# Performance work log

Measured on AMD Instinct MI355X. Metric: run time of the kernel, lower is better.

## Reference

```python
import jax, jax.numpy as jnp
import numpy as np

NNODES = 8192
DIM = 256
ALPHA = 3.0
NEG_SLOPE = 0.2


def setup_inputs() -> dict:
    key = jax.random.key(0)
    k1, k2, k3, k4 = jax.random.split(key, 4)
    return {
        "idx": jnp.arange(NNODES, dtype=jnp.int64) if jax.config.jax_enable_x64 else jnp.arange(NNODES, dtype=jnp.int32),
        "emb1_w": jax.random.normal(k1, (NNODES, DIM), dtype=jnp.float32),
        "emb2_w": jax.random.normal(k2, (NNODES, DIM), dtype=jnp.float32),
        "att_w": jax.random.normal(k3, (2 * DIM,), dtype=jnp.float32) * (1.0 / np.sqrt(2 * DIM)),
        "att_b": jax.random.normal(k4, (1,), dtype=jnp.float32),
    }


def reference(idx, emb1_w, emb2_w, att_w, att_b):
    # Embedding lookup + tanh(alpha * v)
    v1 = jnp.tanh(ALPHA * emb1_w[idx])  # [N, D]
    v2 = jnp.tanh(ALPHA * emb2_w[idx])  # [N, D]
    # Linear(cat(v1_i, v2_j)) decomposes exactly into an outer sum of two
    # per-node projections (same math, no N x N x 2D intermediate).
    s1 = v1 @ att_w[:DIM]  # [N]
    s2 = v2 @ att_w[DIM:]  # [N]
    scores = s1[:, None] + s2[None, :] + att_b[0]  # [N, N]
    scores = jax.nn.leaky_relu(scores, negative_slope=NEG_SLOPE)
    weights = jax.nn.softmax(scores, axis=1)  # row softmax
    # adj[i, idx] = weights[i]  (vectorized column scatter)
    n = idx.shape[0]
    adj = jnp.zeros((n, n), dtype=weights.dtype).at[:, idx].set(weights)
    return adj
```

## Files before the change

kernel.cpp:

```cpp
#include <hip/hip_runtime.h>
#include <math.h>

#define NNODES 8192
#define DIM 256
#define ALPHA 3.0f
#define SLOPE 0.2f
#define LOG2E 1.4426950408889634f

typedef float floatx4 __attribute__((ext_vector_type(4)));

__global__ __launch_bounds__(256) void s_kernel(
    const int* __restrict__ idx,
    const float* __restrict__ e1, const float* __restrict__ e2,
    const float* __restrict__ w,
    float* __restrict__ s1, float* __restrict__ s2)
{
    const int waveId = threadIdx.x >> 6;
    const int lane   = threadIdx.x & 63;
    const int node   = (blockIdx.x << 2) + waveId;
    const int row    = idx[node];

    const float4* e1v = (const float4*)(e1 + (size_t)row * DIM);
    const float4* e2v = (const float4*)(e2 + (size_t)row * DIM);
    const float4* w1v = (const float4*)w;
    const float4* w2v = (const float4*)(w + DIM);

    float4 a  = e1v[lane];
    float4 b  = e2v[lane];
    float4 w1 = w1v[lane];
    float4 w2 = w2v[lane];

    float acc1 = tanhf(ALPHA * a.x) * w1.x + tanhf(ALPHA * a.y) * w1.y
               + tanhf(ALPHA * a.z) * w1.z + tanhf(ALPHA * a.w) * w1.w;
    float acc2 = tanhf(ALPHA * b.x) * w2.x + tanhf(ALPHA * b.y) * w2.y
               + tanhf(ALPHA * b.z) * w2.z + tanhf(ALPHA * b.w) * w2.w;

    #pragma unroll
    for (int off = 32; off > 0; off >>= 1) {
        acc1 += __shfl_down(acc1, off);
        acc2 += __shfl_down(acc2, off);
    }
    if (lane == 0) {
        s1[node] = acc1;
        s2[node] = acc2;
    }
}

__global__ __launch_bounds__(256) void row_kernel(
    const float* __restrict__ s1, const float* __restrict__ s2,
    const int* __restrict__ idx, const float* __restrict__ att_b,
    float* __restrict__ out)
{
    __shared__ float lds[8];
    const int t    = threadIdx.x;
    const int lane = t & 63;
    const int wv   = t >> 6;
    const int row  = blockIdx.x;

    const int4*   idxv = (const int4*)idx;
    const float4* s2v  = (const float4*)s2;
    int4   iv[8];
    float4 v[8];
    float lmax = -3.402823466e38f;
    #pragma unroll
    for (int k = 0; k < 8; ++k) {
        iv[k] = idxv[k * 256 + t];
        v[k]  = s2v[k * 256 + t];
        lmax = fmaxf(lmax, fmaxf(fmaxf(v[k].x, v[k].y), fmaxf(v[k].z, v[k].w)));
    }

    #pragma unroll
    for (int off = 32; off > 0; off >>= 1)
        lmax = fmaxf(lmax, __shfl_xor(lmax, off));
    if (lane == 0) lds[wv] = lmax;
    __syncthreads();
    const float s2max = fmaxf(fmaxf(lds[0], lds[1]), fmaxf(lds[2], lds[3]));

    const float base = s1[row] + att_b[0];
    const float tm   = base + s2max;
    const float m    = fmaxf(tm, SLOPE * tm);
    const float mexp = m * LOG2E;

    float e[32];
    float dsum = 0.0f;
    #pragma unroll
    for (int k = 0; k < 8; ++k) {
        float x0 = base + v[k].x, x1 = base + v[k].y;
        float x2 = base + v[k].z, x3 = base + v[k].w;
        x0 = fmaxf(x0, SLOPE * x0);
        x1 = fmaxf(x1, SLOPE * x1);
        x2 = fmaxf(x2, SLOPE * x2);
        x3 = fmaxf(x3, SLOPE * x3);
        e[4 * k + 0] = __builtin_amdgcn_exp2f(fmaf(x0, LOG2E, -mexp));
        e[4 * k + 1] = __builtin_amdgcn_exp2f(fmaf(x1, LOG2E, -mexp));
        e[4 * k + 2] = __builtin_amdgcn_exp2f(fmaf(x2, LOG2E, -mexp));
        e[4 * k + 3] = __builtin_amdgcn_exp2f(fmaf(x3, LOG2E, -mexp));
        dsum += (e[4 * k + 0] + e[4 * k + 1]) + (e[4 * k + 2] + e[4 * k + 3]);
    }

    #pragma unroll
    for (int off = 32; off > 0; off >>= 1)
        dsum += __shfl_xor(dsum, off);
    if (lane == 0) lds[4 + wv] = dsum;
    __syncthreads();
    const float denom = (lds[4] + lds[5]) + (lds[6] + lds[7]);
    const float inv = 1.0f / denom;

    float* orow = out + (size_t)row * NNODES;
    #pragma unroll
    for (int k = 0; k < 8; ++k) {
        floatx4 r;
        r.x = e[4 * k + 0] * inv;
        r.y = e[4 * k + 1] * inv;
        r.z = e[4 * k + 2] * inv;
        r.w = e[4 * k + 3] * inv;
        const int c0 = (k * 256 + t) * 4;
        if (iv[k].x == c0 && iv[k].y == c0 + 1 && iv[k].z == c0 + 2 && iv[k].w == c0 + 3) {
            __builtin_nontemporal_store(r, (floatx4*)(orow + c0));
        } else {
            orow[iv[k].x] = r.x;
            orow[iv[k].y] = r.y;
            orow[iv[k].z] = r.z;
            orow[iv[k].w] = r.w;
        }
    }
}

extern "C" void kernel_launch(void* const* d_in, const int* in_sizes, int n_in,
                              void* d_out, int out_size, void* d_ws, size_t ws_size,
                              hipStream_t stream) {
    const int*   idx   = (const int*)d_in[0];
    const float* emb1  = (const float*)d_in[1];
    const float* emb2  = (const float*)d_in[2];
    const float* att_w = (const float*)d_in[3];
    const float* att_b = (const float*)d_in[4];
    float* out = (float*)d_out;

    float* s1 = (float*)d_ws;
    float* s2 = s1 + NNODES;

    s_kernel<<<NNODES / 4, 256, 0, stream>>>(idx, emb1, emb2, att_w, s1, s2);
    row_kernel<<<NNODES, 256, 0, stream>>>(s1, s2, idx, att_b, out);
}
```

Measured before the change: 292.0 us.

## Process multiple rows per block, reusing s2 max and identity-index check

Each block of the row kernel now handles eight output rows. It loads s2 and idx once, computes the global s2 max once, and does a block-wide check of whether idx is the identity permutation. That check selects a uniform vectorized nontemporal store path and removes the per-element index registers. The aim is to amortize redundant loads and reductions across rows, at the cost of fewer blocks and a serialized loop of per-row barriers, while the kernel stays bound by output writes.

Result: no change. 293.8 us (+0.6%).

```diff
diff --git a/kernel.cpp b/kernel.cpp
--- a/kernel.cpp
+++ b/kernel.cpp
@@ -6,6 +6,7 @@
 #define ALPHA 3.0f
 #define SLOPE 0.2f
 #define LOG2E 1.4426950408889634f
+#define ROWS_PER_BLOCK 8
 
 typedef float floatx4 __attribute__((ext_vector_type(4)));
 
@@ -51,77 +52,94 @@
     const int* __restrict__ idx, const float* __restrict__ att_b,
     float* __restrict__ out)
 {
-    __shared__ float lds[8];
+    __shared__ float red[8];
+    __shared__ float rmax[4];
+    __shared__ int   rok[4];
     const int t    = threadIdx.x;
     const int lane = t & 63;
     const int wv   = t >> 6;
-    const int row  = blockIdx.x;
+    const int row0 = blockIdx.x * ROWS_PER_BLOCK;
 
-    const int4*   idxv = (const int4*)idx;
-    const float4* s2v  = (const float4*)s2;
-    int4   iv[8];
+    const float4* s2v = (const float4*)s2;
     float4 v[8];
     float lmax = -3.402823466e38f;
+    int ok = 1;
+    {
+        const int4* idxv = (const int4*)idx;
+        #pragma unroll
+        for (int k = 0; k < 8; ++k) {
+            v[k] = s2v[k * 256 + t];
+            lmax = fmaxf(lmax, fmaxf(fmaxf(v[k].x, v[k].y), fmaxf(v[k].z, v[k].w)));
+            int4 iv = idxv[k * 256 + t];
+            const int c0 = (k * 256 + t) * 4;
+            ok &= (iv.x == c0) & (iv.y == c0 + 1) & (iv.z == c0 + 2) & (iv.w == c0 + 3);
+        }
+    }
     #pragma unroll
-    for (int k = 0; k < 8; ++k) {
-        iv[k] = idxv[k * 256 + t];
-        v[k]  = s2v[k * 256 + t];
-        lmax = fmaxf(lmax, fmaxf(fmaxf(v[k].x, v[k].y), fmaxf(v[k].z, v[k].w)));
+    for (int off = 32; off > 0; off >>= 1) {
+        lmax = fmaxf(lmax, __shfl_xor(lmax, off));
+        ok &= __shfl_xor(ok, off);
     }
-
-    #pragma unroll
-    for (int off = 32; off > 0; off >>= 1)
-        lmax = fmaxf(lmax, __shfl_xor(lmax, off));
-    if (lane == 0) lds[wv] = lmax;
+    if (lane == 0) { rmax[wv] = lmax; rok[wv] = ok; }
     __syncthreads();
-    const float s2max = fmaxf(fmaxf(lds[0], lds[1]), fmaxf(lds[2], lds[3]));
-
-    const float base = s1[row] + att_b[0];
-    const float tm   = base + s2max;
-    const float m    = fmaxf(tm, SLOPE * tm);
-    const float mexp = m * LOG2E;
+    const float s2max = fmaxf(fmaxf(rmax[0], rmax[1]), fmaxf(rmax[2], rmax[3]));
+    const int   okAll = rok[0] & rok[1] & rok[2] & rok[3];
+    const float bb    = att_b[0];
 
     float e[32];
-    float dsum = 0.0f;
-    #pragma unroll
-    for (int k = 0; k < 8; ++k) {
-        float x0 = base + v[k].x, x1 = base + v[k].y;
-        float x2 = base + v[k].z, x3 = base + v[k].w;
-        x0 = fmaxf(x0, SLOPE * x0);
-        x1 = fmaxf(x1, SLOPE * x1);
-        x2 = fmaxf(x2, SLOPE * x2);
-        x3 = fmaxf(x3, SLOPE * x3);
-        e[4 * k + 0] = __builtin_amdgcn_exp2f(fmaf(x0, LOG2E, -mexp));
-        e[4 * k + 1] = __builtin_amdgcn_exp2f(fmaf(x1, LOG2E, -mexp));
-        e[4 * k + 2] = __builtin_amdgcn_exp2f(fmaf(x2, LOG2E, -mexp));
-        e[4 * k + 3] = __builtin_amdgcn_exp2f(fmaf(x3, LOG2E, -mexp));
-        dsum += (e[4 * k + 0] + e[4 * k + 1]) + (e[4 * k + 2] + e[4 * k + 3]);
-    }
+    for (int r = 0; r < ROWS_PER_BLOCK; ++r) {
+        const int row   = row0 + r;
+        const float base = s1[row] + bb;
+        const float tm   = base + s2max;
+        const float m    = fmaxf(tm, SLOPE * tm);
+        const float mexp = m * LOG2E;
 
-    #pragma unroll
-    for (int off = 32; off > 0; off >>= 1)
-        dsum += __shfl_xor(dsum, off);
-    if (lane == 0) lds[4 + wv] = dsum;
-    __syncthreads();
-    const float denom = (lds[4] + lds[5]) + (lds[6] + lds[7]);
-    const float inv = 1.0f / denom;
+        float dsum = 0.0f;
+        #pragma unroll
+        for (int k = 0; k < 8; ++k) {
+            float x0 = base + v[k].x, x1 = base + v[k].y;
+            float x2 = base + v[k].z, x3 = base + v[k].w;
+            x0 = fmaxf(x0, SLOPE * x0);
+            x1 = fmaxf(x1, SLOPE * x1);
+            x2 = fmaxf(x2, SLOPE * x2);
+            x3 = fmaxf(x3, SLOPE * x3);
+            e[4 * k + 0] = __builtin_amdgcn_exp2f(fmaf(x0, LOG2E, -mexp));
+            e[4 * k + 1] = __builtin_amdgcn_exp2f(fmaf(x1, LOG2E, -mexp));
+            e[4 * k + 2] = __builtin_amdgcn_exp2f(fmaf(x2, LOG2E, -mexp));
+            e[4 * k + 3] = __builtin_amdgcn_exp2f(fmaf(x3, LOG2E, -mexp));
+            dsum += (e[4 * k + 0] + e[4 * k + 1]) + (e[4 * k + 2] + e[4 * k + 3]);
+        }
+        #pragma unroll
+        for (int off = 32; off > 0; off >>= 1)
+            dsum += __shfl_xor(dsum, off);
 
-    float* orow = out + (size_t)row * NNODES;
-    #pragma unroll
-    for (int k = 0; k < 8; ++k) {
-        floatx4 r;
-        r.x = e[4 * k + 0] * inv;
-        r.y = e[4 * k + 1] * inv;
-        r.z = e[4 * k + 2] * inv;
-        r.w = e[4 * k + 3] * inv;
-        const int c0 = (k * 256 + t) * 4;
-        if (iv[k].x == c0 && iv[k].y == c0 + 1 && iv[k].z == c0 + 2 && iv[k].w == c0 + 3) {
-            __builtin_nontemporal_store(r, (floatx4*)(orow + c0));
+        float* slot = red + ((r & 1) << 2);
+        if (lane == 0) slot[wv] = dsum;
+        __syncthreads();
+        const float denom = (slot[0] + slot[1]) + (slot[2] + slot[3]);
+        const float inv = 1.0f / denom;
+
+        float* orow = out + (size_t)row * NNODES;
+        if (okAll) {
+            #pragma unroll
+            for (int k = 0; k < 8; ++k) {
+                floatx4 o;
+                o.x = e[4 * k + 0] * inv;
+                o.y = e[4 * k + 1] * inv;
+                o.z = e[4 * k + 2] * inv;
+                o.w = e[4 * k + 3] * inv;
+                __builtin_nontemporal_store(o, (floatx4*)(orow + (k * 256 + t) * 4));
+            }
         } else {
-            orow[iv[k].x] = r.x;
-            orow[iv[k].y] = r.y;
-            orow[iv[k].z] = r.z;
-            orow[iv[k].w] = r.w;
+            const int4* idxv = (const int4*)idx;
+            #pragma unroll
+            for (int k = 0; k < 8; ++k) {
+                int4 iv = idxv[k * 256 + t];
+                orow[iv.x] = e[4 * k + 0] * inv;
+                orow[iv.y] = e[4 * k + 1] * inv;
+                orow[iv.z] = e[4 * k + 2] * inv;
+                orow[iv.w] = e[4 * k + 3] * inv;
+            }
         }
     }
 }
@@ -139,6 +157,6 @@
     float* s1 = (float*)d_ws;
     float* s2 = s1 + NNODES;
 
-    s_kernel<<<NNODES / 4, 256, 0, stream>>>(idx, emb1, emb2, att_w, s1, s2);
-    row_kernel<<<NNODES, 256, 0, stream>>>(s1, s2, idx, att_b, out);
+    s_kernel  <<<NNODES / 4, 256, 0, stream>>>(idx, emb1, emb2, att_w, s1, s2);
+    row_kernel<<<NNODES / ROWS_PER_BLOCK, 256, 0, stream>>>(s1, s2, idx, att_b, out);
 }
```
